# Kernel optimization log

Measured on AMD Instinct MI355X. Metric: run time of the kernel, lower is better.

Reference implementation:

```python
import jax, jax.numpy as jnp
import numpy as np

N, T, HIDDEN = 32768, 2048, 128
NF = T // 2 + 1  # rfft bins


def setup_inputs() -> dict:
    key = jax.random.key(0)
    k1, k2, kw1, kw2 = jax.random.split(key, 4)
    x1 = jax.random.normal(k1, (N, T), dtype=jnp.float32)
    x2 = jax.random.normal(k2, (N, T), dtype=jnp.float32)
    # kaiming_uniform (relu): bound = sqrt(6 / fan_in)
    fan1 = 2 * NF
    W1 = jax.random.uniform(kw1, (HIDDEN, fan1), minval=-np.sqrt(6.0 / fan1), maxval=np.sqrt(6.0 / fan1), dtype=jnp.float32)
    b1 = jnp.zeros((HIDDEN,), dtype=jnp.float32)
    W2 = jax.random.uniform(kw2, (T, HIDDEN), minval=-np.sqrt(6.0 / HIDDEN), maxval=np.sqrt(6.0 / HIDDEN), dtype=jnp.float32)
    b2 = jnp.zeros((T,), dtype=jnp.float32)
    return {"x1": x1, "x2": x2, "W1": W1, "b1": b1, "W2": W2, "b2": b2}


def reference(x1, x2, W1, b1, W2, b2):
    # batched rfft replaces the per-sample Python loop
    diff = jnp.fft.rfft(x1, axis=-1) - jnp.fft.rfft(x2, axis=-1)  # [N, NF] complex
    feats = jnp.concatenate([diff.real, diff.imag], axis=-1)       # [N, 2*NF]
    h = jax.nn.relu(feats @ W1.T + b1)                             # [N, HIDDEN]
    out = h @ W2.T + b2                                            # [N, T]
    return jnp.mean(out, axis=-1)                                  # [N]
```

## Files before the change

### kernel.cpp

```cpp
#include <hip/hip_runtime.h>
#include <hip/hip_bf16.h>
#include <math.h>

#define T_LEN   2048
#define NFREQ   1025
#define HID     128
#define NSAMP   32768
#define NIT     64

typedef __attribute__((ext_vector_type(8)))  short short8v;
typedef __attribute__((ext_vector_type(16))) float f32x16;

#define AKG_OFF    0
#define W2BAR_OFF  (1u<<20)
#define B2BAR_OFF  ((1u<<20)+512)
#define PW_OFF     ((1u<<20)+1024)
#define PB_OFF     ((1u<<20)+1024+8192)

__global__ __launch_bounds__(128) void k_w2_partial(const float* __restrict__ W2,
                                                    const float* __restrict__ b2,
                                                    float* __restrict__ pw,
                                                    float* __restrict__ pb) {
    const int b = blockIdx.x;
    const int c = threadIdx.x;
    const int t0 = b * 128;
    float s0 = 0.f, s1 = 0.f, s2 = 0.f, s3 = 0.f;
    #pragma unroll 4
    for (int i = 0; i < 128; i += 4) {
        s0 += W2[(long)(t0 + i + 0) * HID + c];
        s1 += W2[(long)(t0 + i + 1) * HID + c];
        s2 += W2[(long)(t0 + i + 2) * HID + c];
        s3 += W2[(long)(t0 + i + 3) * HID + c];
    }
    pw[b * HID + c] = (s0 + s1) + (s2 + s3);
    float v = b2[t0 + c];
    for (int o = 32; o > 0; o >>= 1) v += __shfl_down(v, o);
    __shared__ float sred[2];
    if ((threadIdx.x & 63) == 0) sred[threadIdx.x >> 6] = v;
    __syncthreads();
    if (threadIdx.x == 0) pb[b] = sred[0] + sred[1];
}

__global__ __launch_bounds__(128) void k_w2_final(const float* __restrict__ pw,
                                                  const float* __restrict__ pb,
                                                  float* __restrict__ w2bar,
                                                  float* __restrict__ b2bar) {
    const int c = threadIdx.x;
    float s = 0.f;
    #pragma unroll
    for (int b = 0; b < 16; ++b) s += pw[b * HID + c];
    w2bar[c] = s * (1.f / (float)T_LEN);
    if (c == 0) {
        float t = 0.f;
        #pragma unroll
        for (int b = 0; b < 16; ++b) t += pb[b];
        *b2bar = t * (1.f / (float)T_LEN);
    }
}

__global__ __launch_bounds__(256) void k_build_At(const float* __restrict__ W1,
                                                  unsigned short* __restrict__ Akg) {
    __shared__ float lW[2 * NFREQ];
    const int k  = blockIdx.x >> 4;
    const int tg = blockIdx.x & 15;
    const int tid = threadIdx.x;
    const float* __restrict__ Wk = W1 + (long)k * (2 * NFREQ);
    for (int i = tid; i < 2 * NFREQ; i += 256) lW[i] = Wk[i];
    __syncthreads();
    const float* __restrict__ lWr = lW;
    const float* __restrict__ lWi = lW + NFREQ;

    const int chunk = tid >> 6;
    const int fh = (tid >> 5) & 1;
    const int tl = tid & 31;
    const int t  = tg * 128 + chunk * 32 + tl;

    const float w = -6.283185307179586f / (float)T_LEN;
    float sr, cr;
    { int ph2 = (2 * t) & (T_LEN - 1); sincosf(w * (float)ph2, &sr, &cr); }
    float zr, zi;
    { int ph = (t * fh) & (T_LEN - 1); sincosf(w * (float)ph, &zi, &zr); }
    float acc = 0.f;
    int f = fh;
    for (int blk = 0; blk < 4; ++blk) {
        #pragma unroll 4
        for (int j = 0; j < 128; ++j) {
            acc = fmaf(lWr[f], zr, acc);
            acc = fmaf(lWi[f], zi, acc);
            float nzr = fmaf(zr, cr, -(zi * sr));
            float nzi = fmaf(zr, sr, zi * cr);
            zr = nzr; zi = nzi;
            f += 2;
        }
        int ph = (t * f) & (T_LEN - 1);
        sincosf(w * (float)ph, &zi, &zr);
    }
    if (fh == 0) {
        acc = fmaf(lWr[1024], zr, acc);
        acc = fmaf(lWi[1024], zi, acc);
    }
    acc += __shfl_xor(acc, 32);

    if (fh == 0) {
        __hip_bfloat16 hb = __float2bfloat16(acc);
        float hf = __bfloat162float(hb);
        __hip_bfloat16 lb = __float2bfloat16(acc - hf);
        const int tile = t >> 5, islot = (t & 31) >> 3, j = t & 7;
        const int shi = islot ^ (k & 7);
        const int slo = (islot ^ 4) ^ (k & 7);
        const long base = (long)tile * 8192 + k * 64 + j;
        Akg[base + shi * 8] = __builtin_bit_cast(unsigned short, hb);
        Akg[base + slo * 8] = __builtin_bit_cast(unsigned short, lb);
    }
}

__global__ __launch_bounds__(512) void k_gemm(const float* __restrict__ x1,
                                              const float* __restrict__ x2,
                                              const unsigned short* __restrict__ Akg,
                                              const float* __restrict__ b1,
                                              const float* __restrict__ w2bar,
                                              const float* __restrict__ b2bar,
                                              float* __restrict__ out) {
    __shared__ __align__(16) unsigned short ak[2][8192];
    __shared__ __align__(16) unsigned short dd[2][8192];
    __shared__ float osum[128];

    const int tid = threadIdx.x;
    const int l   = tid & 63;
    const int w   = tid >> 6;
    const int wm  = w & 3;
    const int wn  = w >> 2;
    const int g   = l >> 5;
    const int m31 = l & 31;
    const long row0 = (long)blockIdx.x * 128;

    const int rs = tid >> 2;
    const int j4 = tid & 3;
    const float* __restrict__ px1 = x1 + (row0 + rs) * T_LEN + j4 * 8;
    const float* __restrict__ px2 = x2 + (row0 + rs) * T_LEN + j4 * 8;
    const unsigned short* __restrict__ pak = Akg + tid * 16;

    const int wr_hi = rs * 64 + ((j4 ^ (rs & 7)) * 8);
    const int ra  = wm * 32 + m31;
    const int rb0 = wn * 64 + m31;
    const int rb1 = wn * 64 + 32 + m31;

    f32x16 acc0, acc1;
    #pragma unroll
    for (int q = 0; q < 16; ++q) { acc0[q] = 0.f; acc1[q] = 0.f; }

    float4 xa0A, xa1A, xb0A, xb1A, xa0B, xa1B, xb0B, xb1B;
    uint4  ak0A, ak1A, ak0B, ak1B;

#define LOADX(S, IT) {                                                      \
        const float* p1_ = px1 + (IT) * 32;                                 \
        const float* p2_ = px2 + (IT) * 32;                                 \
        xa0##S = *(const float4*)(p1_);  xa1##S = *(const float4*)(p1_ + 4);\
        xb0##S = *(const float4*)(p2_);  xb1##S = *(const float4*)(p2_ + 4);\
        const unsigned short* pa_ = pak + (long)(IT) * 8192;                \
        ak0##S = *(const uint4*)(pa_);   ak1##S = *(const uint4*)(pa_ + 8); }

#define STAGE(S, BUF) {                                                     \
        float dv_[8] = {xa0##S.x - xb0##S.x, xa0##S.y - xb0##S.y,           \
                        xa0##S.z - xb0##S.z, xa0##S.w - xb0##S.w,           \
                        xa1##S.x - xb1##S.x, xa1##S.y - xb1##S.y,           \
                        xa1##S.z - xb1##S.z, xa1##S.w - xb1##S.w};          \
        short8v dhv_, dlv_;                                                 \
        _Pragma("unroll")                                                   \
        for (int e = 0; e < 8; ++e) {                                       \
            __hip_bfloat16 hb_ = __float2bfloat16(dv_[e]);                  \
            float lo_ = dv_[e] - __bfloat162float(hb_);                     \
            dhv_[e] = __builtin_bit_cast(short, hb_);                       \
            dlv_[e] = __builtin_bit_cast(short, __float2bfloat16(lo_));     \
        }                                                                   \
        *(short8v*)&dd[BUF][wr_hi]      = dhv_;                             \
        *(short8v*)&dd[BUF][wr_hi ^ 32] = dlv_;                             \
        *(uint4*)&ak[BUF][tid * 16]     = ak0##S;                           \
        *(uint4*)&ak[BUF][tid * 16 + 8] = ak1##S; }

#define LBAR() { asm volatile("s_waitcnt lgkmcnt(0)" ::: "memory");         \
                 __builtin_amdgcn_s_barrier();                              \
                 __builtin_amdgcn_sched_barrier(0); }

#define COMPUTE2(BUF, ACCA, ACCB) {                                         \
        _Pragma("unroll")                                                   \
        for (int kc = 0; kc < 2; ++kc) {                                    \
            const int sa_ = ((2 * kc + g) ^ (ra & 7)) * 8;                  \
            const short8v ah_ = *(const short8v*)&dd[BUF][ra * 64 + sa_];   \
            const short8v al_ = *(const short8v*)&dd[BUF][ra * 64 + (sa_ ^ 32)]; \
            const int sb0_ = ((2 * kc + g) ^ (rb0 & 7)) * 8;                \
            const short8v bh0_ = *(const short8v*)&ak[BUF][rb0 * 64 + sb0_];\
            const short8v bl0_ = *(const short8v*)&ak[BUF][rb0 * 64 + (sb0_ ^ 32)]; \
            const int sb1_ = ((2 * kc + g) ^ (rb1 & 7)) * 8;                \
            const short8v bh1_ = *(const short8v*)&ak[BUF][rb1 * 64 + sb1_];\
            const short8v bl1_ = *(const short8v*)&ak[BUF][rb1 * 64 + (sb1_ ^ 32)]; \
            ACCA = __builtin_amdgcn_mfma_f32_32x32x16_bf16(ah_, bh0_, ACCA, 0, 0, 0); \
            ACCA = __builtin_amdgcn_mfma_f32_32x32x16_bf16(ah_, bl0_, ACCA, 0, 0, 0); \
            ACCA = __builtin_amdgcn_mfma_f32_32x32x16_bf16(al_, bh0_, ACCA, 0, 0, 0); \
            ACCB = __builtin_amdgcn_mfma_f32_32x32x16_bf16(ah_, bh1_, ACCB, 0, 0, 0); \
            ACCB = __builtin_amdgcn_mfma_f32_32x32x16_bf16(ah_, bl1_, ACCB, 0, 0, 0); \
            ACCB = __builtin_amdgcn_mfma_f32_32x32x16_bf16(al_, bh1_, ACCB, 0, 0, 0); \
        } }

    LOADX(A, 0);
    LOADX(B, 1);

    for (int it2 = 0; it2 < NIT / 2; ++it2) {
        const int itA = 2 * it2;
        STAGE(A, 0);
        { int itn = itA + 2; if (itn > NIT - 1) itn = NIT - 1; LOADX(A, itn); }
        LBAR();
        COMPUTE2(0, acc0, acc1);
        STAGE(B, 1);
        { int itn = itA + 3; if (itn > NIT - 1) itn = NIT - 1; LOADX(B, itn); }
        LBAR();
        COMPUTE2(1, acc0, acc1);
    }

#undef LOADX
#undef STAGE
#undef LBAR
#undef COMPUTE2

    float pres[16];
    #pragma unroll
    for (int q = 0; q < 16; ++q) pres[q] = 0.f;
    {
        const int n0 = wn * 64 + m31;
        const float bb0 = b1[n0], wb0 = w2bar[n0];
        const int n1 = wn * 64 + 32 + m31;
        const float bb1v = b1[n1], wb1 = w2bar[n1];
        #pragma unroll
        for (int q = 0; q < 16; ++q) {
            pres[q] += fmaxf(acc0[q] + bb0, 0.f) * wb0;
            pres[q] += fmaxf(acc1[q] + bb1v, 0.f) * wb1;
        }
    }
    #pragma unroll
    for (int q = 0; q < 16; ++q) {
        float s = pres[q];
        s += __shfl_xor(s, 1); s += __shfl_xor(s, 2); s += __shfl_xor(s, 4);
        s += __shfl_xor(s, 8); s += __shfl_xor(s, 16);
        pres[q] = s;
    }
    __syncthreads();
    if (wn == 0 && m31 == 0) {
        #pragma unroll
        for (int q = 0; q < 16; ++q)
            osum[wm * 32 + (q & 3) + 8 * (q >> 2) + 4 * g] = pres[q];
    }
    __syncthreads();
    if (wn == 1 && m31 == 0) {
        const float bb = *b2bar;
        #pragma unroll
        for (int q = 0; q < 16; ++q) {
            const int m = wm * 32 + (q & 3) + 8 * (q >> 2) + 4 * g;
            out[row0 + m] = pres[q] + osum[m] + bb;
        }
    }
}

extern "C" void kernel_launch(void* const* d_in, const int* in_sizes, int n_in,
                              void* d_out, int out_size, void* d_ws, size_t ws_size,
                              hipStream_t stream) {
    const float* x1 = (const float*)d_in[0];
    const float* x2 = (const float*)d_in[1];
    const float* W1 = (const float*)d_in[2];
    const float* b1 = (const float*)d_in[3];
    const float* W2 = (const float*)d_in[4];
    const float* b2 = (const float*)d_in[5];
    float* out = (float*)d_out;

    char* ws = (char*)d_ws;
    unsigned short* Akg = (unsigned short*)(ws + AKG_OFF);
    float* w2bar = (float*)(ws + W2BAR_OFF);
    float* b2bar = (float*)(ws + B2BAR_OFF);
    float* pw    = (float*)(ws + PW_OFF);
    float* pb    = (float*)(ws + PB_OFF);

    hipLaunchKernelGGL(k_w2_partial, dim3(16), dim3(128), 0, stream, W2, b2, pw, pb);
    hipLaunchKernelGGL(k_w2_final,   dim3(1),  dim3(128), 0, stream, pw, pb, w2bar, b2bar);
    hipLaunchKernelGGL(k_build_At,   dim3(2048), dim3(256), 0, stream, W1, Akg);
    hipLaunchKernelGGL(k_gemm,       dim3(NSAMP / 128), dim3(512), 0, stream,
                       x1, x2, Akg, b1, w2bar, b2bar, out);
}
```

Before: 598.5 us.

## Halve GEMM row tile to 64 rows and split HIDDEN across four waves

The fused GEMM block now handles 64 sample rows instead of 128, with the 8 waves laid out as 2 row-groups by 4 hidden-column groups, each holding one 32x32 accumulator. This doubles the grid to 512 blocks, which should spread better across the CUs, and shrinks the per-block LDS footprint and register use. The cost is that the per-block Akg (DFT-weight) tile is loaded twice as often relative to the sample data, raising global and LDS traffic for the weight operand. The epilogue now reduces four partial sums through shared memory instead of two.

```diff
diff --git a/kernel.cpp b/kernel.cpp
--- a/kernel.cpp
+++ b/kernel.cpp
@@ -8,6 +8,7 @@
 #define NSAMP   32768
 #define NIT     64
 
+typedef __attribute__((ext_vector_type(4)))  short short4v;
 typedef __attribute__((ext_vector_type(8)))  short short8v;
 typedef __attribute__((ext_vector_type(16))) float f32x16;
 
@@ -122,59 +123,54 @@
                                               const float* __restrict__ b2bar,
                                               float* __restrict__ out) {
     __shared__ __align__(16) unsigned short ak[2][8192];
-    __shared__ __align__(16) unsigned short dd[2][8192];
-    __shared__ float osum[128];
+    __shared__ __align__(16) unsigned short dd[2][4096];
+    __shared__ float osum[4][64];
 
     const int tid = threadIdx.x;
     const int l   = tid & 63;
     const int w   = tid >> 6;
-    const int wm  = w & 3;
-    const int wn  = w >> 2;
+    const int wn  = w & 3;
+    const int wm  = w >> 2;
     const int g   = l >> 5;
     const int m31 = l & 31;
-    const long row0 = (long)blockIdx.x * 128;
-
-    const int rs = tid >> 2;
-    const int j4 = tid & 3;
-    const float* __restrict__ px1 = x1 + (row0 + rs) * T_LEN + j4 * 8;
-    const float* __restrict__ px2 = x2 + (row0 + rs) * T_LEN + j4 * 8;
+    const long row0 = (long)blockIdx.x * 64;
+
+    const int rs = tid >> 3;
+    const int j8 = tid & 7;
+    const float* __restrict__ px1 = x1 + (row0 + rs) * T_LEN + j8 * 4;
+    const float* __restrict__ px2 = x2 + (row0 + rs) * T_LEN + j8 * 4;
     const unsigned short* __restrict__ pak = Akg + tid * 16;
 
-    const int wr_hi = rs * 64 + ((j4 ^ (rs & 7)) * 8);
+    const int wr_hi = rs * 64 + (((j8 >> 1) ^ (rs & 7)) * 8) + (j8 & 1) * 4;
     const int ra  = wm * 32 + m31;
-    const int rb0 = wn * 64 + m31;
-    const int rb1 = wn * 64 + 32 + m31;
-
-    f32x16 acc0, acc1;
+    const int rb  = wn * 32 + m31;
+
+    f32x16 acc;
     #pragma unroll
-    for (int q = 0; q < 16; ++q) { acc0[q] = 0.f; acc1[q] = 0.f; }
-
-    float4 xa0A, xa1A, xb0A, xb1A, xa0B, xa1B, xb0B, xb1B;
+    for (int q = 0; q < 16; ++q) acc[q] = 0.f;
+
+    float4 xaA, xbA, xaB, xbB;
     uint4  ak0A, ak1A, ak0B, ak1B;
 
 #define LOADX(S, IT) {                                                      \
-        const float* p1_ = px1 + (IT) * 32;                                 \
-        const float* p2_ = px2 + (IT) * 32;                                 \
-        xa0##S = *(const float4*)(p1_);  xa1##S = *(const float4*)(p1_ + 4);\
-        xb0##S = *(const float4*)(p2_);  xb1##S = *(const float4*)(p2_ + 4);\
+        xa##S = *(const float4*)(px1 + (IT) * 32);                          \
+        xb##S = *(const float4*)(px2 + (IT) * 32);                          \
         const unsigned short* pa_ = pak + (long)(IT) * 8192;                \
         ak0##S = *(const uint4*)(pa_);   ak1##S = *(const uint4*)(pa_ + 8); }
 
 #define STAGE(S, BUF) {                                                     \
-        float dv_[8] = {xa0##S.x - xb0##S.x, xa0##S.y - xb0##S.y,           \
-                        xa0##S.z - xb0##S.z, xa0##S.w - xb0##S.w,           \
-                        xa1##S.x - xb1##S.x, xa1##S.y - xb1##S.y,           \
-                        xa1##S.z - xb1##S.z, xa1##S.w - xb1##S.w};          \
-        short8v dhv_, dlv_;                                                 \
+        float dv_[4] = {xa##S.x - xb##S.x, xa##S.y - xb##S.y,               \
+                        xa##S.z - xb##S.z, xa##S.w - xb##S.w};              \
+        short4v dhv_, dlv_;                                                 \
         _Pragma("unroll")                                                   \
-        for (int e = 0; e < 8; ++e) {                                       \
+        for (int e = 0; e < 4; ++e) {                                       \
             __hip_bfloat16 hb_ = __float2bfloat16(dv_[e]);                  \
             float lo_ = dv_[e] - __bfloat162float(hb_);                     \
             dhv_[e] = __builtin_bit_cast(short, hb_);                       \
             dlv_[e] = __builtin_bit_cast(short, __float2bfloat16(lo_));     \
         }                                                                   \
-        *(short8v*)&dd[BUF][wr_hi]      = dhv_;                             \
-        *(short8v*)&dd[BUF][wr_hi ^ 32] = dlv_;                             \
+        *(short4v*)&dd[BUF][wr_hi]      = dhv_;                             \
+        *(short4v*)&dd[BUF][wr_hi ^ 32] = dlv_;                             \
         *(uint4*)&ak[BUF][tid * 16]     = ak0##S;                           \
         *(uint4*)&ak[BUF][tid * 16 + 8] = ak1##S; }
 
@@ -182,24 +178,18 @@
                  __builtin_amdgcn_s_barrier();                              \
                  __builtin_amdgcn_sched_barrier(0); }
 
-#define COMPUTE2(BUF, ACCA, ACCB) {                                         \
+#define COMPUTE(BUF) {                                                      \
         _Pragma("unroll")                                                   \
         for (int kc = 0; kc < 2; ++kc) {                                    \
             const int sa_ = ((2 * kc + g) ^ (ra & 7)) * 8;                  \
             const short8v ah_ = *(const short8v*)&dd[BUF][ra * 64 + sa_];   \
             const short8v al_ = *(const short8v*)&dd[BUF][ra * 64 + (sa_ ^ 32)]; \
-            const int sb0_ = ((2 * kc + g) ^ (rb0 & 7)) * 8;                \
-            const short8v bh0_ = *(const short8v*)&ak[BUF][rb0 * 64 + sb0_];\
-            const short8v bl0_ = *(const short8v*)&ak[BUF][rb0 * 64 + (sb0_ ^ 32)]; \
-            const int sb1_ = ((2 * kc + g) ^ (rb1 & 7)) * 8;                \
-            const short8v bh1_ = *(const short8v*)&ak[BUF][rb1 * 64 + sb1_];\
-            const short8v bl1_ = *(const short8v*)&ak[BUF][rb1 * 64 + (sb1_ ^ 32)]; \
-            ACCA = __builtin_amdgcn_mfma_f32_32x32x16_bf16(ah_, bh0_, ACCA, 0, 0, 0); \
-            ACCA = __builtin_amdgcn_mfma_f32_32x32x16_bf16(ah_, bl0_, ACCA, 0, 0, 0); \
-            ACCA = __builtin_amdgcn_mfma_f32_32x32x16_bf16(al_, bh0_, ACCA, 0, 0, 0); \
-            ACCB = __builtin_amdgcn_mfma_f32_32x32x16_bf16(ah_, bh1_, ACCB, 0, 0, 0); \
-            ACCB = __builtin_amdgcn_mfma_f32_32x32x16_bf16(ah_, bl1_, ACCB, 0, 0, 0); \
-            ACCB = __builtin_amdgcn_mfma_f32_32x32x16_bf16(al_, bh1_, ACCB, 0, 0, 0); \
+            const int sb_ = ((2 * kc + g) ^ (rb & 7)) * 8;                  \
+            const short8v bh_ = *(const short8v*)&ak[BUF][rb * 64 + sb_];   \
+            const short8v bl_ = *(const short8v*)&ak[BUF][rb * 64 + (sb_ ^ 32)]; \
+            acc = __builtin_amdgcn_mfma_f32_32x32x16_bf16(ah_, bh_, acc, 0, 0, 0); \
+            acc = __builtin_amdgcn_mfma_f32_32x32x16_bf16(ah_, bl_, acc, 0, 0, 0); \
+            acc = __builtin_amdgcn_mfma_f32_32x32x16_bf16(al_, bh_, acc, 0, 0, 0); \
         } }
 
     LOADX(A, 0);
@@ -210,31 +200,25 @@
         STAGE(A, 0);
         { int itn = itA + 2; if (itn > NIT - 1) itn = NIT - 1; LOADX(A, itn); }
         LBAR();
-        COMPUTE2(0, acc0, acc1);
+        COMPUTE(0);
         STAGE(B, 1);
         { int itn = itA + 3; if (itn > NIT - 1) itn = NIT - 1; LOADX(B, itn); }
         LBAR();
-        COMPUTE2(1, acc0, acc1);
+        COMPUTE(1);
     }
 
 #undef LOADX
 #undef STAGE
 #undef LBAR
-#undef COMPUTE2
+#undef COMPUTE
 
     float pres[16];
-    #pragma unroll
-    for (int q = 0; q < 16; ++q) pres[q] = 0.f;
     {
-        const int n0 = wn * 64 + m31;
-        const float bb0 = b1[n0], wb0 = w2bar[n0];
-        const int n1 = wn * 64 + 32 + m31;
-        const float bb1v = b1[n1], wb1 = w2bar[n1];
+        const int n = wn * 32 + m31;
+        const float bb1 = b1[n], wb = w2bar[n];
         #pragma unroll
-        for (int q = 0; q < 16; ++q) {
-            pres[q] += fmaxf(acc0[q] + bb0, 0.f) * wb0;
-            pres[q] += fmaxf(acc1[q] + bb1v, 0.f) * wb1;
-        }
+        for (int q = 0; q < 16; ++q)
+            pres[q] = fmaxf(acc[q] + bb1, 0.f) * wb;
     }
     #pragma unroll
     for (int q = 0; q < 16; ++q) {
@@ -243,20 +227,15 @@
         s += __shfl_xor(s, 8); s += __shfl_xor(s, 16);
         pres[q] = s;
     }
-    __syncthreads();
-    if (wn == 0 && m31 == 0) {
+    if (m31 == 0) {
         #pragma unroll
         for (int q = 0; q < 16; ++q)
-            osum[wm * 32 + (q & 3) + 8 * (q >> 2) + 4 * g] = pres[q];
+            osum[wn][wm * 32 + (q & 3) + 8 * (q >> 2) + 4 * g] = pres[q];
     }
     __syncthreads();
-    if (wn == 1 && m31 == 0) {
-        const float bb = *b2bar;
-        #pragma unroll
-        for (int q = 0; q < 16; ++q) {
-            const int m = wm * 32 + (q & 3) + 8 * (q >> 2) + 4 * g;
-            out[row0 + m] = pres[q] + osum[m] + bb;
-        }
+    if (tid < 64) {
+        out[row0 + tid] = osum[0][tid] + osum[1][tid] + osum[2][tid] + osum[3][tid]
+                        + *b2bar;
     }
 }
 
@@ -281,6 +260,6 @@
     hipLaunchKernelGGL(k_w2_partial, dim3(16), dim3(128), 0, stream, W2, b2, pw, pb);
     hipLaunchKernelGGL(k_w2_final,   dim3(1),  dim3(128), 0, stream, pw, pb, w2bar, b2bar);
     hipLaunchKernelGGL(k_build_At,   dim3(2048), dim3(256), 0, stream, W1, Akg);
-    hipLaunchKernelGGL(k_gemm,       dim3(NSAMP / 128), dim3(512), 0, stream,
+    hipLaunchKernelGGL(k_gemm,       dim3(NSAMP / 64), dim3(512), 0, stream,
                        x1, x2, Akg, b1, w2bar, b2bar, out);
 }
```

After: 586.2 us. 1.02x faster.
